# Kernel tuning notes

Hardware: AMD Instinct MI355X
Metric: run time of the kernel (lower is better)

Reference implementation:

```python
import jax, jax.numpy as jnp
import numpy as np

B, T, U = 64, 256, 256
NMEL, PRE, EMB, NF, ENC, DEC, WM, VOCAB = 80, 128, 15, 128, 128, 512, 10, 44
KMAX = 5
_km = np.zeros((3, KMAX), np.float32)
for _i, _k in enumerate([1, 3, 5]):
    _km[_i, (KMAX - _k) // 2:(KMAX - _k) // 2 + _k] = 1.0
KMASK = jnp.asarray(_km)  # [3, KMAX] zero-mask embedding kernels 1/3/5 in width-5 buffers


def _lstm(x, h, c, W, b):
    z = jnp.concatenate([x, h], -1) @ W + b
    i, f, g, o = jnp.split(z, 4, -1)
    cn = jax.nn.sigmoid(f) * c + jax.nn.sigmoid(i) * jnp.tanh(g)
    hn = jax.nn.sigmoid(o) * jnp.tanh(cn)
    return hn, cn


def _conv_stack(x, w, b, residual):
    # x [B,U,Cin]; w [3,KMAX,Cin,NF]; b [3,NF]; multi-kernel-size conv1d stack
    y = 0.0
    for i in range(3):
        wk = w[i] * KMASK[i][:, None, None]
        y = y + jax.lax.conv_general_dilated(x, wk, (1,), 'SAME', dimension_numbers=('NWC', 'WIO', 'NWC')) + b[i]
    y = jax.nn.relu(y)
    return y + x if residual else y


def _forward(text, in_mels, in_mel_mask, text_mask, w_pre1, b_pre1, w_pre2, b_pre2, emb, conv_w0, conv_b0, conv_w1, conv_b1, conv_w2, conv_b2, w_bif, b_bif, w_bib, b_bib, w_attlstm, b_attlstm, w_attproj, b_attproj, w_rnn1, b_rnn1, w_rnn2, b_rnn2, w_out, b_out):
    # mel prenet (two linear layers, dropout keep-prob 1.0 -> identity)
    corr = (in_mels @ w_pre1 + b_pre1) @ w_pre2 + b_pre2  # [T,B,PRE]
    # text encoder: embedding -> conv1d stack -> BiLSTM
    x = jnp.transpose(emb[text], (1, 0, 2))  # [B,U,EMB]
    x = _conv_stack(x, conv_w0, conv_b0, False)
    x = _conv_stack(x, conv_w1, conv_b1, True)
    x = _conv_stack(x, conv_w2, conv_b2, True)
    conv_text = jnp.transpose(x, (1, 0, 2))  # [U,B,NF]
    tm = text_mask[..., None]  # [U,B,1]

    def make_bi(W, bb):
        def f(carry, xs):
            h, c = carry
            xt, mt = xs
            hn, cn = _lstm(xt, h, c, W, bb)
            hn = mt * hn + (1.0 - mt) * h
            cn = mt * cn + (1.0 - mt) * c
            return (hn, cn), hn
        return f

    z0 = (jnp.zeros((B, ENC), jnp.float32), jnp.zeros((B, ENC), jnp.float32))
    _, hf = jax.lax.scan(make_bi(w_bif, b_bif), z0, (conv_text, tm))
    _, hb = jax.lax.scan(make_bi(w_bib, b_bib), z0, (conv_text[::-1], tm[::-1]))
    ctx = jnp.concatenate([hf, hb[::-1]], -1)  # [U,B,2*ENC]

    upos = jnp.arange(U, dtype=jnp.float32)[None, :, None]  # [1,U,1]
    phi_mask = text_mask.T  # [B,U]

    def step(carry, xs):
        att_w, att_k, att_h, att_c, h1, c1, h2, c2 = carry
        corr_t, m_t = xs
        m = m_t[:, None]
        # Gaussian-mixture attention cell (Graves-style, softplus step op)
        ah, ac = _lstm(jnp.concatenate([corr_t, att_w], -1), att_h, att_c, w_attlstm, b_attlstm)
        pr = ah @ w_attproj + b_attproj  # [B,3*WM]
        a_h, b_h, k_h = jnp.split(pr, 3, -1)
        a_t = jax.nn.softplus(a_h)
        b_t = jax.nn.softplus(b_h)
        k_t = att_k + jax.nn.softplus(k_h)  # attention_scale = 1.0
        phi = (a_t[:, None, :] * jnp.exp(-b_t[:, None, :] * (k_t[:, None, :] - upos) ** 2)).sum(-1) * phi_mask  # [B,U]
        w_t = jnp.einsum('bu,ubd->bd', phi, ctx)
        w_t = m * w_t + (1.0 - m) * att_w
        k_t = m * k_t + (1.0 - m) * att_k
        ah = m * ah + (1.0 - m) * att_h
        ac = m * ac + (1.0 - m) * att_c
        h1n, c1n = _lstm(jnp.concatenate([corr_t, w_t, ah], -1), h1, c1, w_rnn1, b_rnn1)
        h1n = m * h1n + (1.0 - m) * h1
        c1n = m * c1n + (1.0 - m) * c1
        h2n, c2n = _lstm(jnp.concatenate([corr_t, w_t, h1n], -1), h2, c2, w_rnn2, b_rnn2)
        h2n = m * h2n + (1.0 - m) * h2
        c2n = m * c2n + (1.0 - m) * c2
        return (w_t, k_t, ah, ac, h1n, c1n, h2n, c2n), h2n

    zf = lambda d: jnp.zeros((B, d), jnp.float32)
    init = (zf(2 * ENC), zf(WM), zf(DEC), zf(DEC), zf(DEC), zf(DEC), zf(DEC), zf(DEC))
    _, outs = jax.lax.scan(step, init, (corr, in_mel_mask))  # outs [T,B,DEC]
    return outs @ w_out + b_out  # [T,B,NMEL]


def setup_inputs():
    key = jax.random.key(0)
    ks = iter(jax.random.split(key, 40))

    def w(shape, s=0.08):
        return jax.random.normal(next(ks), shape, jnp.float32) * s

    z = lambda *s: jnp.zeros(s, jnp.float32)
    return {
        'in_mels': jax.random.normal(next(ks), (T, B, NMEL), jnp.float32),
        'in_mel_mask': jnp.ones((T, B), jnp.float32),
        'text': jax.random.randint(next(ks), (U, B), 0, VOCAB),
        'text_mask': jnp.ones((U, B), jnp.float32),
        'w_pre1': w((NMEL, PRE)), 'b_pre1': z(PRE),
        'w_pre2': w((PRE, PRE)), 'b_pre2': z(PRE),
        'emb': w((VOCAB, EMB), 1.0),
        'conv_w0': w((3, KMAX, EMB, NF)), 'conv_b0': z(3, NF),
        'conv_w1': w((3, KMAX, NF, NF)), 'conv_b1': z(3, NF),
        'conv_w2': w((3, KMAX, NF, NF)), 'conv_b2': z(3, NF),
        'w_bif': w((NF + ENC, 4 * ENC)), 'b_bif': z(4 * ENC),
        'w_bib': w((NF + ENC, 4 * ENC)), 'b_bib': z(4 * ENC),
        'w_attlstm': w((PRE + 2 * ENC + DEC, 4 * DEC)), 'b_attlstm': z(4 * DEC),
        'w_attproj': w((DEC, 3 * WM)), 'b_attproj': z(3 * WM),
        'w_rnn1': w((PRE + 2 * ENC + 2 * DEC, 4 * DEC)), 'b_rnn1': z(4 * DEC),
        'w_rnn2': w((PRE + 2 * ENC + 2 * DEC, 4 * DEC)), 'b_rnn2': z(4 * DEC),
        'w_out': w((DEC, NMEL)), 'b_out': z(NMEL),
    }


def reference(in_mels, in_mel_mask, text, text_mask, w_pre1, b_pre1, w_pre2, b_pre2, emb, conv_w0, conv_b0, conv_w1, conv_b1, conv_w2, conv_b2, w_bif, b_bif, w_bib, b_bib, w_attlstm, b_attlstm, w_attproj, b_attproj, w_rnn1, b_rnn1, w_rnn2, b_rnn2, w_out, b_out):
    return _forward(text, in_mels, in_mel_mask, text_mask, w_pre1, b_pre1, w_pre2, b_pre2, emb, conv_w0, conv_b0, conv_w1, conv_b1, conv_w2, conv_b2, w_bif, b_bif, w_bib, b_bib, w_attlstm, b_attlstm, w_attproj, b_attproj, w_rnn1, b_rnn1, w_rnn2, b_rnn2, w_out, b_out)
```

## Files before the change

### kernel.cpp

```cpp
#include <hip/hip_runtime.h>
#include <math.h>

constexpr int NB    = 64;
constexpr int NT    = 256;
constexpr int NU    = 256;
constexpr int NMELc = 80;
constexpr int PREc  = 128;
constexpr int EMBc  = 15;
constexpr int NFc   = 128;
constexpr int ENCc  = 128;
constexpr int DECc  = 512;
constexpr int WMc   = 10;
constexpr int AKS   = 16;
constexpr size_t WSZ = (size_t)116 * 128 * 512;

using bf16x8 = __attribute__((ext_vector_type(8))) short;
using us8    = __attribute__((ext_vector_type(8))) unsigned short;
using f32x4  = __attribute__((ext_vector_type(4))) float;

__device__ __forceinline__ float sigm(float x) { return 1.0f / (1.0f + expf(-x)); }
__device__ __forceinline__ float softplusf(float x) { return fmaxf(x, 0.0f) + log1pf(expf(-fabsf(x))); }
__device__ __forceinline__ unsigned short f2bf(float f) {
  unsigned u = __builtin_bit_cast(unsigned, f);
  return (unsigned short)((u + 0x7FFFu + ((u >> 16) & 1u)) >> 16);
}
__device__ __forceinline__ float bf2f(unsigned short h) {
  return __builtin_bit_cast(float, (unsigned)h << 16);
}
__device__ __forceinline__ float ldF(const float* p) {
  return __hip_atomic_load(p, __ATOMIC_RELAXED, __HIP_MEMORY_SCOPE_AGENT);
}
__device__ __forceinline__ void stF(float* p, float v) {
  __hip_atomic_store(p, v, __ATOMIC_RELAXED, __HIP_MEMORY_SCOPE_AGENT);
}
__device__ __forceinline__ float2 ldF2(const float* p) {
  unsigned long long u = __hip_atomic_load((const unsigned long long*)p, __ATOMIC_RELAXED,
                                           __HIP_MEMORY_SCOPE_AGENT);
  return __builtin_bit_cast(float2, u);
}
__device__ __forceinline__ unsigned ldU(const unsigned* p) {
  return __hip_atomic_load(p, __ATOMIC_RELAXED, __HIP_MEMORY_SCOPE_AGENT);
}
__device__ __forceinline__ void stU(unsigned* p, unsigned v) {
  __hip_atomic_store(p, v, __ATOMIC_RELAXED, __HIP_MEMORY_SCOPE_AGENT);
}

template <int K, int N, int RB>
__global__ void k_dense(const float* __restrict__ X, const float* __restrict__ W,
                        const float* __restrict__ bias, float* __restrict__ Y, int R) {
  __shared__ float xs[RB][K];
  int r0 = blockIdx.x * RB;
  int tid = threadIdx.x;
  for (int idx = tid; idx < RB * K; idx += 128) {
    int r = idx / K, k = idx % K;
    xs[r][k] = (r0 + r < R) ? X[(size_t)(r0 + r) * K + k] : 0.0f;
  }
  __syncthreads();
  int j = tid;
  if (j >= N) return;
  float acc[RB];
#pragma unroll
  for (int r = 0; r < RB; ++r) acc[r] = 0.f;
  for (int k = 0; k < K; ++k) {
    float w = W[(size_t)k * N + j];
#pragma unroll
    for (int r = 0; r < RB; ++r) acc[r] += xs[r][k] * w;
  }
  float bj = bias[j];
  for (int r = 0; r < RB; ++r)
    if (r0 + r < R) Y[(size_t)(r0 + r) * N + j] = acc[r] + bj;
}

__global__ void k_embed(const int* __restrict__ text, const float* __restrict__ emb,
                        float* __restrict__ out) {
  int idx = blockIdx.x * blockDim.x + threadIdx.x;
  if (idx >= NB * NU * EMBc) return;
  int c = idx % EMBc;
  int bu = idx / EMBc;
  int u = bu % NU, b = bu / NU;
  out[idx] = emb[text[u * NB + b] * EMBc + c];
}

template <int CIN>
__global__ void k_weff(const float* __restrict__ w, const float* __restrict__ bb,
                       float* __restrict__ weff, float* __restrict__ beff) {
  int idx = blockIdx.x * blockDim.x + threadIdx.x;
  const int tot = 5 * CIN * NFc;
  if (idx < tot) {
    int f = idx % NFc;
    int tc = idx / NFc;
    int c = tc % CIN, t = tc / CIN;
// ... 120 lines not shown
      __syncthreads();
    }
    int upos = d ? (NU - 1 - u) : u;
#pragma unroll
    for (int e = 0; e < 2; ++e) {
      int idx = 2 * tid + e;
      int bi = idx >> 7, j = idx & 127;
      int b = b0 + bi;
      float zi = zs[bi][j], zf = zs[bi][128 + j], zg = zs[bi][256 + j], zo = zs[bi][384 + j];
      float cp = creg[e], hp = hs[bi][j];
      float cn = sigm(zf) * cp + sigm(zi) * tanhf(zg);
      float hn = sigm(zo) * tanhf(cn);
      float mt = text_mask[upos * NB + b];
      hn = mt * hn + (1.f - mt) * hp;
      cn = mt * cn + (1.f - mt) * cp;
      creg[e] = cn;
      hs[bi][j] = hn;
      ctx[((size_t)upos * NB + b) * 256 + d * 128 + j] = hn;
    }
    __syncthreads();
  }
}

__global__ __launch_bounds__(256) void k_wcvt(const float* __restrict__ w1,
                                              const float* __restrict__ wa,
                                              const float* __restrict__ w2,
                                              unsigned short* __restrict__ Wpk) {
  int ktg = blockIdx.x;
  int ntg = blockIdx.y;
  const float* W;
  int ktl;
  if (ktg < 44) { W = w1; ktl = ktg; }
  else if (ktg < 72) { W = wa; ktl = ktg - 44; }
  else { W = w2; ktl = ktg - 72; }
  int tid = threadIdx.x;
  for (int p = 0; p < 8; ++p) {
    int idx = p * 256 + tid;
    int ntl = idx >> 6, l = idx & 63;
    int nt = ntg * 32 + ntl;
    us8 vh, vl;
#pragma unroll
    for (int j = 0; j < 8; ++j) {
      float wv = W[(size_t)(ktl * 32 + (l >> 4) * 8 + j) * 2048 + nt * 16 + (l & 15)];
      unsigned short h = f2bf(wv);
      vh[j] = h;
      vl[j] = f2bf(wv - bf2f(h));
    }
    size_t o = (((size_t)ktg * 128 + nt) * 64 + l) * 8;
    *(us8*)(Wpk + o) = vh;
    *(us8*)(Wpk + WSZ + o) = vl;
  }
}

struct DecMp {
  const float* corr;
  const unsigned short* Wpk;
  const float *mel_mask, *text_mask, *ctx;
  const float *b_att, *b_rnn1, *b_rnn2, *w_proj, *b_proj;
  float *aw, *ak, *ah, *ac, *h1, *c1, *c2, *outs, *zerob;
  float* zX;
  unsigned* flags;
};

__device__ __forceinline__ void wait_flags(const unsigned* flags, int base, unsigned target) {
  int tid = threadIdx.x;
  for (;;) {
    bool ok = true;
    if (tid < 128) {
      int f = (tid < 64) ? (base + tid) : (192 + base + (tid - 64));
      ok = (ldU(&flags[f]) >= target);
    }
    if (__syncthreads_and(ok)) break;
    __builtin_amdgcn_s_sleep(8);
  }
}

__device__ __forceinline__ void do_gateM(const float* zX, int clo, int chi, const float* bias,
                                         const float* cprev, const float* hprev, bool zfirst,
                                         const float* mm, float* hout, float* cout, int b, int j) {
  float2 zi = *(const float2*)(bias + j);
  float2 zf = *(const float2*)(bias + 512 + j);
  float2 zg = *(const float2*)(bias + 1024 + j);
  float2 zo = *(const float2*)(bias + 1536 + j);
  for (int c = clo; c <= chi; ++c) {
    const float* q = zX + ((size_t)c * NB + b) * 2048 + j;
    float2 a = ldF2(q), f2 = ldF2(q + 512), g2 = ldF2(q + 1024), o2 = ldF2(q + 1536);
    zi.x += a.x; zi.y += a.y;
    zf.x += f2.x; zf.y += f2.y;
    zg.x += g2.x; zg.y += g2.y;
    zo.x += o2.x; zo.y += o2.y;
  }
  float2 cp = zfirst ? make_float2(0.f, 0.f) : *(const float2*)(cprev + (size_t)b * 512 + j);
  float2 hp = zfirst ? make_float2(0.f, 0.f) : *(const float2*)(hprev + (size_t)b * 512 + j);
  float m = mm[b];
  float cnx = sigm(zf.x) * cp.x + sigm(zi.x) * tanhf(zg.x);
  float cny = sigm(zf.y) * cp.y + sigm(zi.y) * tanhf(zg.y);
  float hnx = sigm(zo.x) * tanhf(cnx);
  float hny = sigm(zo.y) * tanhf(cny);
  *(float2*)(hout + (size_t)b * 512 + j) =
      make_float2(m * hnx + (1.f - m) * hp.x, m * hny + (1.f - m) * hp.y);
  *(float2*)(cout + (size_t)b * 512 + j) =
      make_float2(m * cnx + (1.f - m) * cp.x, m * cny + (1.f - m) * cp.y);
}

__global__ __launch_bounds__(256) void k_decM(DecMp P, int i) {
  __shared__ __align__(16) unsigned short xsh[32][360];
  __shared__ __align__(16) unsigned short xsl[32][360];
  int tid = threadIdx.x, bid = blockIdx.x;
  if (bid < 384) {
    int bg = bid / 192, r = bid % 192, c = r >> 4, nc = r & 15;
    int g, ktg0, nkt, k0;
    if (c < 4)      { g = 0; ktg0 = c * 11;            nkt = 11; k0 = c * 352; }
    else if (c < 8) { g = 1; ktg0 = 44 + (c - 4) * 7;  nkt = 7;  k0 = (c - 4) * 224; }
    else            { g = 2; ktg0 = 72 + (c - 8) * 11; nkt = 11; k0 = (c - 8) * 352; }
    int s = (g == 0) ? (i - 1) : (g == 1 ? i : (i - 2));
    if (s >= 0 && s < NT) {
      const float* p0 = P.corr + (size_t)s * NB * PREc;
      const float *p1, *p2, *p3;
      int s1, s2_, s3;
      if (g == 1) {
        bool z = (s == 0);
        int pp = (s - 1) & 1;
        p1 = z ? P.zerob : P.aw + (size_t)pp * NB * 256; s1 = z ? 0 : 256;
        p2 = z ? P.zerob : P.ah + (size_t)pp * NB * DECc; s2_ = z ? 0 : DECc;
        p3 = P.zerob; s3 = 0;
      } else if (g == 0) {
        int pp = s & 1;
        p1 = P.aw + (size_t)pp * NB * 256; s1 = 256;
        p2 = P.ah + (size_t)pp * NB * DECc; s2_ = DECc;
        bool z = (s == 0);
        p3 = z ? P.zerob : P.h1 + (size_t)((s - 1) & 1) * NB * DECc; s3 = z ? 0 : DECc;
      } else {
        int pp = s & 1;
        p1 = P.aw + (size_t)pp * NB * 256; s1 = 256;
        p2 = P.h1 + (size_t)pp * NB * DECc; s2_ = DECc;
        bool z = (s == 0);
        p3 = z ? P.zerob : P.outs + (size_t)(s - 1) * NB * DECc; s3 = z ? 0 : DECc;
      }
      int klen = nkt * 32;
      for (int idx = tid; idx < klen; idx += 256) {
        int k = k0 + idx;
#pragma unroll 4
        for (int bi = 0; bi < 32; ++bi) {
          int b = bg * 32 + bi;
          float v;
          int kx = k;
          if (kx < PREc)
            v = p0[(size_t)b * PREc + kx];
          else {
            kx -= PREc;
            if (kx < 256)
              v = p1[(size_t)b * s1 + kx];
            else {
              kx -= 256;
              if (kx < DECc)
                v = p2[(size_t)b * s2_ + kx];
              else
                v = p3[(size_t)b * s3 + (kx - DECc)];
            }
          }
          unsigned short h = f2bf(v);
          xsh[bi][idx] = h;
          xsl[bi][idx] = f2bf(v - bf2f(h));
        }
      }
      __syncthreads();
      int w = tid >> 6, lane = tid & 63;
      const unsigned short* wb0 =
          P.Wpk + (((size_t)ktg0 * 128 + (size_t)(nc * 8 + w * 2)) * 64 + lane) * 8;
      f32x4 acc[2][2];
#pragma unroll
      for (int m = 0; m < 2; ++m)
#pragma unroll
        for (int t = 0; t < 2; ++t) acc[m][t] = f32x4{0.f, 0.f, 0.f, 0.f};
      int arow0 = lane & 15, acol = (lane >> 4) * 8;
      for (int kt = 0; kt < nkt; ++kt) {
        bf16x8 ah0 = *(const bf16x8*)&xsh[arow0][kt * 32 + acol];
        bf16x8 ah1 = *(const bf16x8*)&xsh[16 + arow0][kt * 32 + acol];
        bf16x8 al0 = *(const bf16x8*)&xsl[arow0][kt * 32 + acol];
        bf16x8 al1 = *(const bf16x8*)&xsl[16 + arow0][kt * 32 + acol];
        const unsigned short* wp = wb0 + (size_t)kt * 65536;
        bf16x8 b0h = *(const bf16x8*)(wp);
        bf16x8 b1h = *(const bf16x8*)(wp + 512);
        bf16x8 b0l = *(const bf16x8*)(wp + WSZ);
        bf16x8 b1l = *(const bf16x8*)(wp + WSZ + 512);
        acc[0][0] = __builtin_amdgcn_mfma_f32_16x16x32_bf16(ah0, b0h, acc[0][0], 0, 0, 0);
        acc[0][1] = __builtin_amdgcn_mfma_f32_16x16x32_bf16(ah0, b1h, acc[0][1], 0, 0, 0);
        acc[1][0] = __builtin_amdgcn_mfma_f32_16x16x32_bf16(ah1, b0h, acc[1][0], 0, 0, 0);
        acc[1][1] = __builtin_amdgcn_mfma_f32_16x16x32_bf16(ah1, b1h, acc[1][1], 0, 0, 0);
        acc[0][0] = __builtin_amdgcn_mfma_f32_16x16x32_bf16(al0, b0h, acc[0][0], 0, 0, 0);
        acc[0][1] = __builtin_amdgcn_mfma_f32_16x16x32_bf16(al0, b1h, acc[0][1], 0, 0, 0);
        acc[1][0] = __builtin_amdgcn_mfma_f32_16x16x32_bf16(al1, b0h, acc[1][0], 0, 0, 0);
        acc[1][1] = __builtin_amdgcn_mfma_f32_16x16x32_bf16(al1, b1h, acc[1][1], 0, 0, 0);
        acc[0][0] = __builtin_amdgcn_mfma_f32_16x16x32_bf16(ah0, b0l, acc[0][0], 0, 0, 0);
        acc[0][1] = __builtin_amdgcn_mfma_f32_16x16x32_bf16(ah0, b1l, acc[0][1], 0, 0, 0);
        acc[1][0] = __builtin_amdgcn_mfma_f32_16x16x32_bf16(ah1, b0l, acc[1][0], 0, 0, 0);
        acc[1][1] = __builtin_amdgcn_mfma_f32_16x16x32_bf16(ah1, b1l, acc[1][1], 0, 0, 0);
      }
#pragma unroll
      for (int m = 0; m < 2; ++m)
#pragma unroll
        for (int t = 0; t < 2; ++t) {
          int brow = bg * 32 + m * 16 + (lane >> 4) * 4;
          int col = nc * 128 + (w * 2 + t) * 16 + (lane & 15);
          float* zb = P.zX + ((size_t)c * NB + brow) * 2048 + col;
#pragma unroll
          for (int rr = 0; rr < 4; ++rr) stF(zb + (size_t)rr * 2048, acc[m][t][rr]);
        }
    }
    __syncthreads();
    if (tid == 0) stU(&P.flags[bid], (unsigned)(i + 1));
    return;
  }
  int wb = bid - 384;
  unsigned target = (unsigned)(i + 1);
  if (wb < 64) {
    int s = i - 1;
    if (s < 0 || s >= NT) return;
    wait_flags(P.flags, 0, target);
    bool z = (s == 0);
    do_gateM(P.zX, 0, 3, P.b_rnn1,
             z ? P.zerob : P.c1 + (size_t)((s - 1) & 1) * NB * 512,
             z ? P.zerob : P.h1 + (size_t)((s - 1) & 1) * NB * 512, z,
             P.mel_mask + (size_t)s * NB,
             P.h1 + (size_t)(s & 1) * NB * 512,
             P.c1 + (size_t)(s & 1) * NB * 512, wb, 2 * tid);
    return;
  }
  if (wb < 128) {
    int s = i - 2;
    if (s < 0 || s >= NT) return;
    wait_flags(P.flags, 128, target);
    bool z = (s == 0);
    do_gateM(P.zX, 8, 11, P.b_rnn2,
             z ? P.zerob : P.c2 + (size_t)((s - 1) & 1) * NB * 512,
             z ? P.zerob : P.outs + (size_t)(s - 1) * NB * 512, z,
             P.mel_mask + (size_t)s * NB,
             P.outs + (size_t)s * NB * 512,
             P.c2 + (size_t)(s & 1) * NB * 512, wb - 64, 2 * tid);
    return;
  }
  int s = i;
  if (s >= NT) return;
  wait_flags(P.flags, 64, target);
  int b = wb - 128;
  float* sh = (float*)&xsh[0][0];
  float* ah_s = sh;
  float* red_s = sh + 512;
  float* pr_s = sh + 768;
  float* abk = sh + 800;
  float* phi_s = sh + 896;
  float m = P.mel_mask[(size_t)s * NB + b];
  bool z = (s == 0);
  int pp = (s - 1) & 1;
  {
    int j = 2 * tid;
    float2 zi = *(const float2*)(P.b_att + j);
    float2 zf = *(const float2*)(P.b_att + 512 + j);
    float2 zg = *(const float2*)(P.b_att + 1024 + j);
    float2 zo = *(const float2*)(P.b_att + 1536 + j);
    for (int cc = 4; cc <= 7; ++cc) {
      const float* q = P.zX + ((size_t)cc * NB + b) * 2048 + j;
      float2 a = ldF2(q), f2 = ldF2(q + 512), g2 = ldF2(q + 1024), o2 = ldF2(q + 1536);
      zi.x += a.x; zi.y += a.y;
      zf.x += f2.x; zf.y += f2.y;
      zg.x += g2.x; zg.y += g2.y;
      zo.x += o2.x; zo.y += o2.y;
    }
    float2 cp = z ? make_float2(0.f, 0.f)
                  : *(const float2*)(P.ac + (size_t)pp * NB * 512 + (size_t)b * 512 + j);
    float2 hp = z ? make_float2(0.f, 0.f)
                  : *(const float2*)(P.ah + (size_t)pp * NB * 512 + (size_t)b * 512 + j);
    float cnx = sigm(zf.x) * cp.x + sigm(zi.x) * tanhf(zg.x);
    float cny = sigm(zf.y) * cp.y + sigm(zi.y) * tanhf(zg.y);
    float hrx = sigm(zo.x) * tanhf(cnx);
    float hry = sigm(zo.y) * tanhf(cny);
    ah_s[j] = hrx;
    ah_s[j + 1] = hry;
    *(float2*)(P.ah + (size_t)(s & 1) * NB * 512 + (size_t)b * 512 + j) =
        make_float2(m * hrx + (1.f - m) * hp.x, m * hry + (1.f - m) * hp.y);
    *(float2*)(P.ac + (size_t)(s & 1) * NB * 512 + (size_t)b * 512 + j) =
        make_float2(m * cnx + (1.f - m) * cp.x, m * cny + (1.f - m) * cp.y);
  }
  __syncthreads();
  {
    int cc2 = tid & 31, ch = tid >> 5;
    float ssum = 0.f;
    if (cc2 < 30)
      for (int k = ch * 64; k < ch * 64 + 64; ++k) ssum += ah_s[k] * P.w_proj[k * 30 + cc2];
    red_s[ch * 32 + cc2] = ssum;
  }
  __syncthreads();
  if (tid < 30) {
    float ssum = P.b_proj[tid];
    for (int ch = 0; ch < 8; ++ch) ssum += red_s[ch * 32 + tid];
    pr_s[tid] = ssum;
  }
  __syncthreads();
  if (tid < WMc) {
    float kp = z ? 0.f : P.ak[(size_t)pp * NB * AKS + (size_t)b * AKS + tid];
    float a_t = softplusf(pr_s[tid]);
    float b_t = softplusf(pr_s[WMc + tid]);
    float k_t = kp + softplusf(pr_s[2 * WMc + tid]);
    abk[tid] = a_t;
    abk[32 + tid] = b_t;
    abk[64 + tid] = k_t;
    P.ak[(size_t)(s & 1) * NB * AKS + (size_t)b * AKS + tid] = m * k_t + (1.f - m) * kp;
  }
  __syncthreads();
  {
    int u = tid;
    float ssum = 0.f;
#pragma unroll
    for (int gg = 0; gg < WMc; ++gg) {
      float dd = abk[64 + gg] - (float)u;
      ssum += abk[gg] * expf(-abk[32 + gg] * dd * dd);
    }
    phi_s[u] = ssum * P.text_mask[u * NB + b];
  }
  __syncthreads();
  {
    int dcol = tid;
    float ssum = 0.f;
#pragma unroll 8
    for (int u = 0; u < NU; ++u)
      ssum += phi_s[u] * __builtin_nontemporal_load(P.ctx + ((size_t)u * NB + b) * 256 + dcol);
    float wprev = z ? 0.f : P.aw[(size_t)pp * NB * 256 + (size_t)b * 256 + dcol];
    P.aw[(size_t)(s & 1) * NB * 256 + (size_t)b * 256 + dcol] = m * ssum + (1.f - m) * wprev;
  }
}

extern "C" void kernel_launch(void* const* d_in, const int* in_sizes, int n_in,
                              void* d_out, int out_size, void* d_ws, size_t ws_size,
                              hipStream_t stream) {
  const float* in_mels = (const float*)d_in[0];
  const float* mel_mask = (const float*)d_in[1];
  const int* text = (const int*)d_in[2];
  const float* text_mask = (const float*)d_in[3];
  const float* w_pre1 = (const float*)d_in[4];
  const float* b_pre1 = (const float*)d_in[5];
  const float* w_pre2 = (const float*)d_in[6];
  const float* b_pre2 = (const float*)d_in[7];
  const float* emb = (const float*)d_in[8];
  const float* conv_w0 = (const float*)d_in[9];
  const float* conv_b0 = (const float*)d_in[10];
  const float* conv_w1 = (const float*)d_in[11];
  const float* conv_b1 = (const float*)d_in[12];
  const float* conv_w2 = (const float*)d_in[13];
  const float* conv_b2 = (const float*)d_in[14];
  const float* w_bif = (const float*)d_in[15];
  const float* b_bif = (const float*)d_in[16];
  const float* w_bib = (const float*)d_in[17];
  const float* b_bib = (const float*)d_in[18];
  const float* w_att = (const float*)d_in[19];
  const float* b_att = (const float*)d_in[20];
  const float* w_proj = (const float*)d_in[21];
  const float* b_proj = (const float*)d_in[22];
  const float* w_rnn1 = (const float*)d_in[23];
  const float* b_rnn1 = (const float*)d_in[24];
  const float* w_rnn2 = (const float*)d_in[25];
  const float* b_rnn2 = (const float*)d_in[26];
  const float* w_outp = (const float*)d_in[27];
  const float* b_outp = (const float*)d_in[28];

  float* ws = (float*)d_ws;
  size_t off = 0;
  auto alloc = [&](size_t n) {
    float* p = ws + off;
    off += (n + 63) & ~(size_t)63;
    return p;
  };
  float* corr = alloc((size_t)NT * NB * PREc);
  float* embx = alloc((size_t)NB * NU * EMBc);
  float* wpkR = alloc(WSZ);
  float* zX = alloc((size_t)12 * NB * 2048);
  float* ctx = alloc((size_t)NU * NB * 2 * ENCc);
  float* convbuf = alloc((size_t)NB * NU * NFc);
  float* aw = alloc((size_t)2 * NB * 2 * ENCc);
  float* ak = alloc((size_t)2 * NB * AKS);
  float* ah = alloc((size_t)2 * NB * DECc);
  float* ac = alloc((size_t)2 * NB * DECc);
  float* h1 = alloc((size_t)2 * NB * DECc);
  float* c1 = alloc((size_t)2 * NB * DECc);
  float* c2 = alloc((size_t)2 * NB * DECc);
  float* outs = alloc((size_t)NT * NB * DECc);
  float* weff0 = alloc((size_t)5 * EMBc * NFc);
  float* beff0 = alloc(NFc);
  float* weff1 = alloc((size_t)5 * NFc * NFc);
  float* beff1 = alloc(NFc);
  float* weff2 = alloc((size_t)5 * NFc * NFc);
  float* beff2 = alloc(NFc);
  float* zerob = alloc(1024);
  float* flagsf = alloc(512);
  unsigned* flags = (unsigned*)flagsf;

  unsigned short* Wpk = (unsigned short*)wpkR;
  _Float16* zx = (_Float16*)outs;
  float* tmp = wpkR;
  float* convA = wpkR;
  float* convB = ctx;

  hipMemsetAsync(zerob, 0, 1024 * sizeof(float), stream);
  hipMemsetAsync(flags, 0, 512 * sizeof(unsigned), stream);

  k_dense<NMELc, PREc, 8><<<NT * NB / 8, 128, 0, stream>>>(in_mels, w_pre1, b_pre1, tmp, NT * NB);
  k_dense<PREc, PREc, 8><<<NT * NB / 8, 128, 0, stream>>>(tmp, w_pre2, b_pre2, corr, NT * NB);

  k_embed<<<(NB * NU * EMBc + 255) / 256, 256, 0, stream>>>(text, emb, embx);
  k_weff<EMBc><<<(5 * EMBc * NFc + 255) / 256, 256, 0, stream>>>(conv_w0, conv_b0, weff0, beff0);
  k_weff<NFc><<<(5 * NFc * NFc + 255) / 256, 256, 0, stream>>>(conv_w1, conv_b1, weff1, beff1);
  k_weff<NFc><<<(5 * NFc * NFc + 255) / 256, 256, 0, stream>>>(conv_w2, conv_b2, weff2, beff2);
  k_conv<EMBc, false><<<dim3(NU / 8, NB), 128, 0, stream>>>(embx, weff0, beff0, convB);
  k_conv<NFc, true><<<dim3(NU / 8, NB), 128, 0, stream>>>(convB, weff1, beff1, convA);
  k_conv<NFc, true><<<dim3(NU / 8, NB), 128, 0, stream>>>(convA, weff2, beff2, convbuf);

  k_wcvt<<<dim3(116, 4), 256, 0, stream>>>(w_rnn1, w_att, w_rnn2, Wpk);

  k_zx<<<dim3(512, 8), 512, 0, stream>>>(w_bif, b_bif, w_bib, b_bib, convbuf, zx);
  k_encP2<<<32, 256, 0, stream>>>(w_bif, w_bib, zx, text_mask, ctx);

  DecMp M;
  M.corr = corr; M.Wpk = Wpk;
  M.mel_mask = mel_mask; M.text_mask = text_mask; M.ctx = ctx;
  M.b_att = b_att; M.b_rnn1 = b_rnn1; M.b_rnn2 = b_rnn2;
  M.w_proj = w_proj; M.b_proj = b_proj;
  M.aw = aw; M.ak = ak; M.ah = ah; M.ac = ac;
  M.h1 = h1; M.c1 = c1; M.c2 = c2; M.outs = outs; M.zerob = zerob;
  M.zX = zX; M.flags = flags;
  for (int i = 0; i <= NT + 1; ++i) {
    k_decM<<<576, 256, 0, stream>>>(M, i);
  }

  k_dense<DECc, NMELc, 8><<<NT * NB / 8, 128, 0, stream>>>(outs, w_outp, b_outp, (float*)d_out,
                                                           NT * NB);
}
```

Before: 13.05 ms.

## Replace per-step decoder launches with one persistent kernel using flag-based sync

The 258 separate decoder kernel launches are folded into a single persistent kernel of 512 blocks. Each block loops over all timesteps and coordinates with per-batch-group and per-batch flags in global memory. GEMM blocks, gate blocks (rnn1 and rnn2 merged into one block per batch row) and attention blocks each spin on the producer flags they depend on. This removes launch overhead and inter-kernel bubbles, but needs every block co-resident (launch_bounds with 2 blocks per CU) and adds spin-wait and atomic-load traffic.

```diff
diff --git a/kernel.cpp b/kernel.cpp
--- a/kernel.cpp
+++ b/kernel.cpp
@@ -37,6 +37,10 @@
   unsigned long long u = __hip_atomic_load((const unsigned long long*)p, __ATOMIC_RELAXED,
                                            __HIP_MEMORY_SCOPE_AGENT);
   return __builtin_bit_cast(float2, u);
+}
+__device__ __forceinline__ void stF2(float* p, float2 v) {
+  __hip_atomic_store((unsigned long long*)p, __builtin_bit_cast(unsigned long long, v),
+                     __ATOMIC_RELAXED, __HIP_MEMORY_SCOPE_AGENT);
 }
 __device__ __forceinline__ unsigned ldU(const unsigned* p) {
   return __hip_atomic_load(p, __ATOMIC_RELAXED, __HIP_MEMORY_SCOPE_AGENT);
@@ -263,58 +267,17 @@
   }
 }
 
-struct DecMp {
+struct DecPp {
   const float* corr;
   const unsigned short* Wpk;
   const float *mel_mask, *text_mask, *ctx;
   const float *b_att, *b_rnn1, *b_rnn2, *w_proj, *b_proj;
   float *aw, *ak, *ah, *ac, *h1, *c1, *c2, *outs, *zerob;
   float* zX;
-  unsigned* flags;
+  unsigned *fa, *fbatt, *fbg;
 };
 
-__device__ __forceinline__ void wait_flags(const unsigned* flags, int base, unsigned target) {
-  int tid = threadIdx.x;
-  for (;;) {
-    bool ok = true;
-    if (tid < 128) {
-      int f = (tid < 64) ? (base + tid) : (192 + base + (tid - 64));
-      ok = (ldU(&flags[f]) >= target);
-    }
-    if (__syncthreads_and(ok)) break;
-    __builtin_amdgcn_s_sleep(8);
-  }
-}
-
-__device__ __forceinline__ void do_gateM(const float* zX, int clo, int chi, const float* bias,
-                                         const float* cprev, const float* hprev, bool zfirst,
-                                         const float* mm, float* hout, float* cout, int b, int j) {
-  float2 zi = *(const float2*)(bias + j);
-  float2 zf = *(const float2*)(bias + 512 + j);
-  float2 zg = *(const float2*)(bias + 1024 + j);
-  float2 zo = *(const float2*)(bias + 1536 + j);
-  for (int c = clo; c <= chi; ++c) {
-    const float* q = zX + ((size_t)c * NB + b) * 2048 + j;
-    float2 a = ldF2(q), f2 = ldF2(q + 512), g2 = ldF2(q + 1024), o2 = ldF2(q + 1536);
-    zi.x += a.x; zi.y += a.y;
-    zf.x += f2.x; zf.y += f2.y;
-    zg.x += g2.x; zg.y += g2.y;
-    zo.x += o2.x; zo.y += o2.y;
-  }
-  float2 cp = zfirst ? make_float2(0.f, 0.f) : *(const float2*)(cprev + (size_t)b * 512 + j);
-  float2 hp = zfirst ? make_float2(0.f, 0.f) : *(const float2*)(hprev + (size_t)b * 512 + j);
-  float m = mm[b];
-  float cnx = sigm(zf.x) * cp.x + sigm(zi.x) * tanhf(zg.x);
-  float cny = sigm(zf.y) * cp.y + sigm(zi.y) * tanhf(zg.y);
-  float hnx = sigm(zo.x) * tanhf(cnx);
-  float hny = sigm(zo.y) * tanhf(cny);
-  *(float2*)(hout + (size_t)b * 512 + j) =
-      make_float2(m * hnx + (1.f - m) * hp.x, m * hny + (1.f - m) * hp.y);
-  *(float2*)(cout + (size_t)b * 512 + j) =
-      make_float2(m * cnx + (1.f - m) * cp.x, m * cny + (1.f - m) * cp.y);
-}
-
-__global__ __launch_bounds__(256) void k_decM(DecMp P, int i) {
+__global__ __launch_bounds__(256, 2) void k_decP3(DecPp P) {
   __shared__ __align__(16) unsigned short xsh[32][360];
   __shared__ __align__(16) unsigned short xsl[32][360];
   int tid = threadIdx.x, bid = blockIdx.x;
@@ -324,220 +287,302 @@
     if (c < 4)      { g = 0; ktg0 = c * 11;            nkt = 11; k0 = c * 352; }
     else if (c < 8) { g = 1; ktg0 = 44 + (c - 4) * 7;  nkt = 7;  k0 = (c - 4) * 224; }
     else            { g = 2; ktg0 = 72 + (c - 8) * 11; nkt = 11; k0 = (c - 8) * 352; }
-    int s = (g == 0) ? (i - 1) : (g == 1 ? i : (i - 2));
-    if (s >= 0 && s < NT) {
-      const float* p0 = P.corr + (size_t)s * NB * PREc;
-      const float *p1, *p2, *p3;
-      int s1, s2_, s3;
-      if (g == 1) {
-        bool z = (s == 0);
-        int pp = (s - 1) & 1;
-        p1 = z ? P.zerob : P.aw + (size_t)pp * NB * 256; s1 = z ? 0 : 256;
-        p2 = z ? P.zerob : P.ah + (size_t)pp * NB * DECc; s2_ = z ? 0 : DECc;
-        p3 = P.zerob; s3 = 0;
-      } else if (g == 0) {
-        int pp = s & 1;
-        p1 = P.aw + (size_t)pp * NB * 256; s1 = 256;
-        p2 = P.ah + (size_t)pp * NB * DECc; s2_ = DECc;
-        bool z = (s == 0);
-        p3 = z ? P.zerob : P.h1 + (size_t)((s - 1) & 1) * NB * DECc; s3 = z ? 0 : DECc;
-      } else {
-        int pp = s & 1;
-        p1 = P.aw + (size_t)pp * NB * 256; s1 = 256;
-        p2 = P.h1 + (size_t)pp * NB * DECc; s2_ = DECc;
-        bool z = (s == 0);
-        p3 = z ? P.zerob : P.outs + (size_t)(s - 1) * NB * DECc; s3 = z ? 0 : DECc;
-      }
-      int klen = nkt * 32;
-      for (int idx = tid; idx < klen; idx += 256) {
-        int k = k0 + idx;
+    int b0 = bg * 32;
+    int w = tid >> 6, lane = tid & 63;
+    const unsigned short* wb0 =
+        P.Wpk + (((size_t)ktg0 * 128 + (size_t)(nc * 8 + w * 2)) * 64 + lane) * 8;
+    int arow0 = lane & 15, acol = (lane >> 4) * 8;
+    for (int i = 0; i <= NT + 1; ++i) {
+      unsigned ta, tg;
+      if (g == 0)      { ta = (unsigned)i; tg = (unsigned)i; }
+      else if (g == 1) { ta = (unsigned)i; tg = 0u; }
+      else             { ta = (i > 0) ? (unsigned)(i - 1) : 0u; tg = (unsigned)i; }
+      for (;;) {
+        bool ok = true;
+        if (tid < 32) ok = (ldU(&P.fbatt[b0 + tid]) >= ta);
+        else if (tid < 64) ok = (ldU(&P.fbg[b0 + tid - 32]) >= tg);
+        if (__syncthreads_and(ok)) break;
+        __builtin_amdgcn_s_sleep(16);
+      }
+      int s = (g == 0) ? (i - 1) : (g == 1 ? i : (i - 2));
+      if (s >= 0 && s < NT) {
+        const float* p0 = P.corr + (size_t)s * NB * PREc;
+        const float *p1, *p2, *p3;
+        int s1, s2_, s3;
+        if (g == 1) {
+          bool z = (s == 0);
+          int pp = (s - 1) & 1;
+          p1 = z ? P.zerob : P.aw + (size_t)pp * NB * 256; s1 = z ? 0 : 256;
+          p2 = z ? P.zerob : P.ah + (size_t)pp * NB * DECc; s2_ = z ? 0 : DECc;
+          p3 = P.zerob; s3 = 0;
+        } else if (g == 0) {
+          int pp = s & 1;
+          p1 = P.aw + (size_t)pp * NB * 256; s1 = 256;
+          p2 = P.ah + (size_t)pp * NB * DECc; s2_ = DECc;
+          bool z = (s == 0);
+          p3 = z ? P.zerob : P.h1 + (size_t)((s - 1) & 1) * NB * DECc; s3 = z ? 0 : DECc;
+        } else {
+          int pp = s & 1;
+          p1 = P.aw + (size_t)pp * NB * 256; s1 = 256;
+          p2 = P.h1 + (size_t)pp * NB * DECc; s2_ = DECc;
+          bool z = (s == 0);
+          p3 = z ? P.zerob : P.outs + (size_t)(s - 1) * NB * DECc; s3 = z ? 0 : DECc;
+        }
+        int klen = nkt * 32;
+        for (int idx = tid; idx < klen; idx += 256) {
+          int k = k0 + idx;
 #pragma unroll 4
-        for (int bi = 0; bi < 32; ++bi) {
-          int b = bg * 32 + bi;
-          float v;
-          int kx = k;
-          if (kx < PREc)
-            v = p0[(size_t)b * PREc + kx];
-          else {
-            kx -= PREc;
-            if (kx < 256)
-              v = p1[(size_t)b * s1 + kx];
+          for (int bi = 0; bi < 32; ++bi) {
+            int b = b0 + bi;
+            float v;
+            int kx = k;
+            if (kx < PREc)
+              v = p0[(size_t)b * PREc + kx];
             else {
-              kx -= 256;
-              if (kx < DECc)
-                v = p2[(size_t)b * s2_ + kx];
-              else
-                v = p3[(size_t)b * s3 + (kx - DECc)];
+              kx -= PREc;
+              if (kx < 256)
+                v = ldF(p1 + (size_t)b * s1 + kx);
+              else {
+                kx -= 256;
+                if (kx < DECc)
+                  v = ldF(p2 + (size_t)b * s2_ + kx);
+                else
+                  v = ldF(p3 + (size_t)b * s3 + (kx - DECc));
+              }
             }
+            unsigned short h = f2bf(v);
+            xsh[bi][idx] = h;
+            xsl[bi][idx] = f2bf(v - bf2f(h));
           }
-          unsigned short h = f2bf(v);
-          xsh[bi][idx] = h;
-          xsl[bi][idx] = f2bf(v - bf2f(h));
-        }
-      }
-      __syncthreads();
-      int w = tid >> 6, lane = tid & 63;
-      const unsigned short* wb0 =
-          P.Wpk + (((size_t)ktg0 * 128 + (size_t)(nc * 8 + w * 2)) * 64 + lane) * 8;
-      f32x4 acc[2][2];
-#pragma unroll
-      for (int m = 0; m < 2; ++m)
-#pragma unroll
-        for (int t = 0; t < 2; ++t) acc[m][t] = f32x4{0.f, 0.f, 0.f, 0.f};
-      int arow0 = lane & 15, acol = (lane >> 4) * 8;
-      for (int kt = 0; kt < nkt; ++kt) {
-        bf16x8 ah0 = *(const bf16x8*)&xsh[arow0][kt * 32 + acol];
-        bf16x8 ah1 = *(const bf16x8*)&xsh[16 + arow0][kt * 32 + acol];
-        bf16x8 al0 = *(const bf16x8*)&xsl[arow0][kt * 32 + acol];
-        bf16x8 al1 = *(const bf16x8*)&xsl[16 + arow0][kt * 32 + acol];
-        const unsigned short* wp = wb0 + (size_t)kt * 65536;
-        bf16x8 b0h = *(const bf16x8*)(wp);
-        bf16x8 b1h = *(const bf16x8*)(wp + 512);
-        bf16x8 b0l = *(const bf16x8*)(wp + WSZ);
-        bf16x8 b1l = *(const bf16x8*)(wp + WSZ + 512);
-        acc[0][0] = __builtin_amdgcn_mfma_f32_16x16x32_bf16(ah0, b0h, acc[0][0], 0, 0, 0);
-        acc[0][1] = __builtin_amdgcn_mfma_f32_16x16x32_bf16(ah0, b1h, acc[0][1], 0, 0, 0);
-        acc[1][0] = __builtin_amdgcn_mfma_f32_16x16x32_bf16(ah1, b0h, acc[1][0], 0, 0, 0);
-        acc[1][1] = __builtin_amdgcn_mfma_f32_16x16x32_bf16(ah1, b1h, acc[1][1], 0, 0, 0);
-        acc[0][0] = __builtin_amdgcn_mfma_f32_16x16x32_bf16(al0, b0h, acc[0][0], 0, 0, 0);
-        acc[0][1] = __builtin_amdgcn_mfma_f32_16x16x32_bf16(al0, b1h, acc[0][1], 0, 0, 0);
-        acc[1][0] = __builtin_amdgcn_mfma_f32_16x16x32_bf16(al1, b0h, acc[1][0], 0, 0, 0);
-        acc[1][1] = __builtin_amdgcn_mfma_f32_16x16x32_bf16(al1, b1h, acc[1][1], 0, 0, 0);
-        acc[0][0] = __builtin_amdgcn_mfma_f32_16x16x32_bf16(ah0, b0l, acc[0][0], 0, 0, 0);
-        acc[0][1] = __builtin_amdgcn_mfma_f32_16x16x32_bf16(ah0, b1l, acc[0][1], 0, 0, 0);
-        acc[1][0] = __builtin_amdgcn_mfma_f32_16x16x32_bf16(ah1, b0l, acc[1][0], 0, 0, 0);
-        acc[1][1] = __builtin_amdgcn_mfma_f32_16x16x32_bf16(ah1, b1l, acc[1][1], 0, 0, 0);
-      }
-#pragma unroll
-      for (int m = 0; m < 2; ++m)
-#pragma unroll
-        for (int t = 0; t < 2; ++t) {
-          int brow = bg * 32 + m * 16 + (lane >> 4) * 4;
-          int col = nc * 128 + (w * 2 + t) * 16 + (lane & 15);
-          float* zb = P.zX + ((size_t)c * NB + brow) * 2048 + col;
-#pragma unroll
-          for (int rr = 0; rr < 4; ++rr) stF(zb + (size_t)rr * 2048, acc[m][t][rr]);
-        }
+        }
+        __syncthreads();
+        f32x4 acc[2][2];
+#pragma unroll
+        for (int m = 0; m < 2; ++m)
+#pragma unroll
+          for (int t = 0; t < 2; ++t) acc[m][t] = f32x4{0.f, 0.f, 0.f, 0.f};
+        for (int kt = 0; kt < nkt; ++kt) {
+          bf16x8 ah0 = *(const bf16x8*)&xsh[arow0][kt * 32 + acol];
+          bf16x8 ah1 = *(const bf16x8*)&xsh[16 + arow0][kt * 32 + acol];
+          bf16x8 al0 = *(const bf16x8*)&xsl[arow0][kt * 32 + acol];
+          bf16x8 al1 = *(const bf16x8*)&xsl[16 + arow0][kt * 32 + acol];
+          const unsigned short* wp = wb0 + (size_t)kt * 65536;
+          bf16x8 b0h = *(const bf16x8*)(wp);
+          bf16x8 b1h = *(const bf16x8*)(wp + 512);
+          bf16x8 b0l = *(const bf16x8*)(wp + WSZ);
+          bf16x8 b1l = *(const bf16x8*)(wp + WSZ + 512);
+          acc[0][0] = __builtin_amdgcn_mfma_f32_16x16x32_bf16(ah0, b0h, acc[0][0], 0, 0, 0);
+          acc[0][1] = __builtin_amdgcn_mfma_f32_16x16x32_bf16(ah0, b1h, acc[0][1], 0, 0, 0);
+          acc[1][0] = __builtin_amdgcn_mfma_f32_16x16x32_bf16(ah1, b0h, acc[1][0], 0, 0, 0);
+          acc[1][1] = __builtin_amdgcn_mfma_f32_16x16x32_bf16(ah1, b1h, acc[1][1], 0, 0, 0);
+          acc[0][0] = __builtin_amdgcn_mfma_f32_16x16x32_bf16(al0, b0h, acc[0][0], 0, 0, 0);
+          acc[0][1] = __builtin_amdgcn_mfma_f32_16x16x32_bf16(al0, b1h, acc[0][1], 0, 0, 0);
+          acc[1][0] = __builtin_amdgcn_mfma_f32_16x16x32_bf16(al1, b0h, acc[1][0], 0, 0, 0);
+          acc[1][1] = __builtin_amdgcn_mfma_f32_16x16x32_bf16(al1, b1h, acc[1][1], 0, 0, 0);
+          acc[0][0] = __builtin_amdgcn_mfma_f32_16x16x32_bf16(ah0, b0l, acc[0][0], 0, 0, 0);
+          acc[0][1] = __builtin_amdgcn_mfma_f32_16x16x32_bf16(ah0, b1l, acc[0][1], 0, 0, 0);
+          acc[1][0] = __builtin_amdgcn_mfma_f32_16x16x32_bf16(ah1, b0l, acc[1][0], 0, 0, 0);
+          acc[1][1] = __builtin_amdgcn_mfma_f32_16x16x32_bf16(ah1, b1l, acc[1][1], 0, 0, 0);
+        }
+#pragma unroll
+        for (int m = 0; m < 2; ++m)
+#pragma unroll
+          for (int t = 0; t < 2; ++t) {
+            int brow = b0 + m * 16 + (lane >> 4) * 4;
+            int col = nc * 128 + (w * 2 + t) * 16 + (lane & 15);
+            float* zb = P.zX + ((size_t)c * NB + brow) * 2048 + col;
+#pragma unroll
+            for (int rr = 0; rr < 4; ++rr) stF(zb + (size_t)rr * 2048, acc[m][t][rr]);
+          }
+      }
+      __syncthreads();
+      if (tid == 0) stU(&P.fa[bid], (unsigned)(i + 1));
+    }
+    return;
+  }
+  int wb = bid - 384;
+  if (wb < 64) {
+    int b = wb;
+    int bg = b >> 5;
+    for (int i = 0; i <= NT + 1; ++i) {
+      for (;;) {
+        bool ok = true;
+        if (tid < 128) {
+          int idx = tid >> 4;
+          int cc = (idx < 4) ? idx : (idx + 4);
+          ok = (ldU(&P.fa[bg * 192 + cc * 16 + (tid & 15)]) >= (unsigned)(i + 1));
+        }
+        if (__syncthreads_and(ok)) break;
+        __builtin_amdgcn_s_sleep(16);
+      }
+      int j = 2 * tid;
+      {
+        int s = i - 1;
+        if (s >= 0 && s < NT) {
+          bool z = (s == 0);
+          const float* cprev = z ? P.zerob : P.c1 + (size_t)((s - 1) & 1) * NB * 512;
+          const float* hprev = z ? P.zerob : P.h1 + (size_t)((s - 1) & 1) * NB * 512;
+          float2 zi = *(const float2*)(P.b_rnn1 + j);
+          float2 zf = *(const float2*)(P.b_rnn1 + 512 + j);
+          float2 zg = *(const float2*)(P.b_rnn1 + 1024 + j);
+          float2 zo = *(const float2*)(P.b_rnn1 + 1536 + j);
+          for (int cc = 0; cc <= 3; ++cc) {
+            const float* q = P.zX + ((size_t)cc * NB + b) * 2048 + j;
+            float2 a = ldF2(q), f2 = ldF2(q + 512), g2 = ldF2(q + 1024), o2 = ldF2(q + 1536);
+            zi.x += a.x; zi.y += a.y;
+            zf.x += f2.x; zf.y += f2.y;
+            zg.x += g2.x; zg.y += g2.y;
+            zo.x += o2.x; zo.y += o2.y;
+          }
+          float2 cp = z ? make_float2(0.f, 0.f) : ldF2(cprev + (size_t)b * 512 + j);
+          float2 hp = z ? make_float2(0.f, 0.f) : ldF2(hprev + (size_t)b * 512 + j);
+          float m = P.mel_mask[(size_t)s * NB + b];
+          float cnx = sigm(zf.x) * cp.x + sigm(zi.x) * tanhf(zg.x);
+          float cny = sigm(zf.y) * cp.y + sigm(zi.y) * tanhf(zg.y);
+          float hnx = sigm(zo.x) * tanhf(cnx);
+          float hny = sigm(zo.y) * tanhf(cny);
+          stF2(P.h1 + (size_t)(s & 1) * NB * 512 + (size_t)b * 512 + j,
+               make_float2(m * hnx + (1.f - m) * hp.x, m * hny + (1.f - m) * hp.y));
+          stF2(P.c1 + (size_t)(s & 1) * NB * 512 + (size_t)b * 512 + j,
+               make_float2(m * cnx + (1.f - m) * cp.x, m * cny + (1.f - m) * cp.y));
+        }
+      }
+      {
+        int s = i - 2;
+        if (s >= 0 && s < NT) {
+          bool z = (s == 0);
+          const float* cprev = z ? P.zerob : P.c2 + (size_t)((s - 1) & 1) * NB * 512;
+          const float* hprev = z ? P.zerob : P.outs + (size_t)(s - 1) * NB * 512;
+          float2 zi = *(const float2*)(P.b_rnn2 + j);
+          float2 zf = *(const float2*)(P.b_rnn2 + 512 + j);
+          float2 zg = *(const float2*)(P.b_rnn2 + 1024 + j);
+          float2 zo = *(const float2*)(P.b_rnn2 + 1536 + j);
+          for (int cc = 8; cc <= 11; ++cc) {
+            const float* q = P.zX + ((size_t)cc * NB + b) * 2048 + j;
+            float2 a = ldF2(q), f2 = ldF2(q + 512), g2 = ldF2(q + 1024), o2 = ldF2(q + 1536);
+            zi.x += a.x; zi.y += a.y;
+            zf.x += f2.x; zf.y += f2.y;
+            zg.x += g2.x; zg.y += g2.y;
+            zo.x += o2.x; zo.y += o2.y;
+          }
+          float2 cp = z ? make_float2(0.f, 0.f) : ldF2(cprev + (size_t)b * 512 + j);
+          float2 hp = z ? make_float2(0.f, 0.f) : ldF2(hprev + (size_t)b * 512 + j);
+          float m = P.mel_mask[(size_t)s * NB + b];
+          float cnx = sigm(zf.x) * cp.x + sigm(zi.x) * tanhf(zg.x);
+          float cny = sigm(zf.y) * cp.y + sigm(zi.y) * tanhf(zg.y);
+          float hnx = sigm(zo.x) * tanhf(cnx);
+          float hny = sigm(zo.y) * tanhf(cny);
+          stF2(P.outs + (size_t)s * NB * 512 + (size_t)b * 512 + j,
+               make_float2(m * hnx + (1.f - m) * hp.x, m * hny + (1.f - m) * hp.y));
+          stF2(P.c2 + (size_t)(s & 1) * NB * 512 + (size_t)b * 512 + j,
+               make_float2(m * cnx + (1.f - m) * cp.x, m * cny + (1.f - m) * cp.y));
+        }
+      }
+      __syncthreads();
+      if (tid == 0) stU(&P.fbg[b], (unsigned)(i + 1));
+    }
+    return;
+  }
+  int b = wb - 64;
+  int bg = b >> 5;
+  float* sh = (float*)&xsh[0][0];
+  for (int i = 0; i <= NT + 1; ++i) {
+    for (;;) {
+      bool ok = true;
+      if (tid < 64)
+        ok = (ldU(&P.fa[bg * 192 + (4 + (tid >> 4)) * 16 + (tid & 15)]) >= (unsigned)(i + 1));
+      if (__syncthreads_and(ok)) break;
+      __builtin_amdgcn_s_sleep(16);
+    }
+    int s = i;
+    if (s < NT) {
+      float* ah_s = sh;
+      float* red_s = sh + 512;
+      float* pr_s = sh + 768;
+      float* abk = sh + 800;
+      float* phi_s = sh + 896;
+      float m = P.mel_mask[(size_t)s * NB + b];
+      bool z = (s == 0);
+      int pp = (s - 1) & 1;
+      {
+        int j = 2 * tid;
+        float2 zi = *(const float2*)(P.b_att + j);
+        float2 zf = *(const float2*)(P.b_att + 512 + j);
+        float2 zg = *(const float2*)(P.b_att + 1024 + j);
+        float2 zo = *(const float2*)(P.b_att + 1536 + j);
+        for (int cc = 4; cc <= 7; ++cc) {
+          const float* q = P.zX + ((size_t)cc * NB + b) * 2048 + j;
+          float2 a = ldF2(q), f2 = ldF2(q + 512), g2 = ldF2(q + 1024), o2 = ldF2(q + 1536);
+          zi.x += a.x; zi.y += a.y;
+          zf.x += f2.x; zf.y += f2.y;
+          zg.x += g2.x; zg.y += g2.y;
+          zo.x += o2.x; zo.y += o2.y;
+        }
+        float2 cp = z ? make_float2(0.f, 0.f)
+                      : ldF2(P.ac + (size_t)pp * NB * 512 + (size_t)b * 512 + j);
+        float2 hp = z ? make_float2(0.f, 0.f)
+                      : ldF2(P.ah + (size_t)pp * NB * 512 + (size_t)b * 512 + j);
+        float cnx = sigm(zf.x) * cp.x + sigm(zi.x) * tanhf(zg.x);
+        float cny = sigm(zf.y) * cp.y + sigm(zi.y) * tanhf(zg.y);
+        float hrx = sigm(zo.x) * tanhf(cnx);
+        float hry = sigm(zo.y) * tanhf(cny);
+        ah_s[j] = hrx;
+        ah_s[j + 1] = hry;
+        stF2(P.ah + (size_t)(s & 1) * NB * 512 + (size_t)b * 512 + j,
+             make_float2(m * hrx + (1.f - m) * hp.x, m * hry + (1.f - m) * hp.y));
+        stF2(P.ac + (size_t)(s & 1) * NB * 512 + (size_t)b * 512 + j,
+             make_float2(m * cnx + (1.f - m) * cp.x, m * cny + (1.f - m) * cp.y));
+      }
+      __syncthreads();
+      {
+        int cc2 = tid & 31, ch = tid >> 5;
+        float ssum = 0.f;
+        if (cc2 < 30)
+          for (int k = ch * 64; k < ch * 64 + 64; ++k) ssum += ah_s[k] * P.w_proj[k * 30 + cc2];
+        red_s[ch * 32 + cc2] = ssum;
+      }
+      __syncthreads();
+      if (tid < 30) {
+        float ssum = P.b_proj[tid];
+        for (int ch = 0; ch < 8; ++ch) ssum += red_s[ch * 32 + tid];
+        pr_s[tid] = ssum;
+      }
+      __syncthreads();
+      if (tid < WMc) {
+        float kp = z ? 0.f : ldF(P.ak + (size_t)pp * NB * AKS + (size_t)b * AKS + tid);
+        float a_t = softplusf(pr_s[tid]);
+        float b_t = softplusf(pr_s[WMc + tid]);
+        float k_t = kp + softplusf(pr_s[2 * WMc + tid]);
+        abk[tid] = a_t;
+        abk[32 + tid] = b_t;
+        abk[64 + tid] = k_t;
+        stF(P.ak + (size_t)(s & 1) * NB * AKS + (size_t)b * AKS + tid, m * k_t + (1.f - m) * kp);
+      }
+      __syncthreads();
+      {
+        int u = tid;
+        float ssum = 0.f;
+#pragma unroll
+        for (int gg = 0; gg < WMc; ++gg) {
+          float dd = abk[64 + gg] - (float)u;
+          ssum += abk[gg] * expf(-abk[32 + gg] * dd * dd);
+        }
+        phi_s[u] = ssum * P.text_mask[u * NB + b];
+      }
+      __syncthreads();
+      {
+        int dcol = tid;
+        float ssum = 0.f;
+#pragma unroll 8
+        for (int u = 0; u < NU; ++u)
+          ssum += phi_s[u] * __builtin_nontemporal_load(P.ctx + ((size_t)u * NB + b) * 256 + dcol);
+        float wprev = z ? 0.f : ldF(P.aw + (size_t)pp * NB * 256 + (size_t)b * 256 + dcol);
+        stF(P.aw + (size_t)(s & 1) * NB * 256 + (size_t)b * 256 + dcol,
+            m * ssum + (1.f - m) * wprev);
+      }
     }
     __syncthreads();
-    if (tid == 0) stU(&P.flags[bid], (unsigned)(i + 1));
-    return;
-  }
-  int wb = bid - 384;
-  unsigned target = (unsigned)(i + 1);
-  if (wb < 64) {
-    int s = i - 1;
-    if (s < 0 || s >= NT) return;
-    wait_flags(P.flags, 0, target);
-    bool z = (s == 0);
-    do_gateM(P.zX, 0, 3, P.b_rnn1,
-             z ? P.zerob : P.c1 + (size_t)((s - 1) & 1) * NB * 512,
-             z ? P.zerob : P.h1 + (size_t)((s - 1) & 1) * NB * 512, z,
-             P.mel_mask + (size_t)s * NB,
-             P.h1 + (size_t)(s & 1) * NB * 512,
-             P.c1 + (size_t)(s & 1) * NB * 512, wb, 2 * tid);
-    return;
-  }
-  if (wb < 128) {
-    int s = i - 2;
-    if (s < 0 || s >= NT) return;
-    wait_flags(P.flags, 128, target);
-    bool z = (s == 0);
-    do_gateM(P.zX, 8, 11, P.b_rnn2,
-             z ? P.zerob : P.c2 + (size_t)((s - 1) & 1) * NB * 512,
-             z ? P.zerob : P.outs + (size_t)(s - 1) * NB * 512, z,
-             P.mel_mask + (size_t)s * NB,
-             P.outs + (size_t)s * NB * 512,
-             P.c2 + (size_t)(s & 1) * NB * 512, wb - 64, 2 * tid);
-    return;
-  }
-  int s = i;
-  if (s >= NT) return;
-  wait_flags(P.flags, 64, target);
-  int b = wb - 128;
-  float* sh = (float*)&xsh[0][0];
-  float* ah_s = sh;
-  float* red_s = sh + 512;
-  float* pr_s = sh + 768;
-  float* abk = sh + 800;
-  float* phi_s = sh + 896;
-  float m = P.mel_mask[(size_t)s * NB + b];
-  bool z = (s == 0);
-  int pp = (s - 1) & 1;
-  {
-    int j = 2 * tid;
-    float2 zi = *(const float2*)(P.b_att + j);
-    float2 zf = *(const float2*)(P.b_att + 512 + j);
-    float2 zg = *(const float2*)(P.b_att + 1024 + j);
-    float2 zo = *(const float2*)(P.b_att + 1536 + j);
-    for (int cc = 4; cc <= 7; ++cc) {
-      const float* q = P.zX + ((size_t)cc * NB + b) * 2048 + j;
-      float2 a = ldF2(q), f2 = ldF2(q + 512), g2 = ldF2(q + 1024), o2 = ldF2(q + 1536);
-      zi.x += a.x; zi.y += a.y;
-      zf.x += f2.x; zf.y += f2.y;
-      zg.x += g2.x; zg.y += g2.y;
-      zo.x += o2.x; zo.y += o2.y;
-    }
-    float2 cp = z ? make_float2(0.f, 0.f)
-                  : *(const float2*)(P.ac + (size_t)pp * NB * 512 + (size_t)b * 512 + j);
-    float2 hp = z ? make_float2(0.f, 0.f)
-                  : *(const float2*)(P.ah + (size_t)pp * NB * 512 + (size_t)b * 512 + j);
-    float cnx = sigm(zf.x) * cp.x + sigm(zi.x) * tanhf(zg.x);
-    float cny = sigm(zf.y) * cp.y + sigm(zi.y) * tanhf(zg.y);
-    float hrx = sigm(zo.x) * tanhf(cnx);
-    float hry = sigm(zo.y) * tanhf(cny);
-    ah_s[j] = hrx;
-    ah_s[j + 1] = hry;
-    *(float2*)(P.ah + (size_t)(s & 1) * NB * 512 + (size_t)b * 512 + j) =
-        make_float2(m * hrx + (1.f - m) * hp.x, m * hry + (1.f - m) * hp.y);
-    *(float2*)(P.ac + (size_t)(s & 1) * NB * 512 + (size_t)b * 512 + j) =
-        make_float2(m * cnx + (1.f - m) * cp.x, m * cny + (1.f - m) * cp.y);
-  }
-  __syncthreads();
-  {
-    int cc2 = tid & 31, ch = tid >> 5;
-    float ssum = 0.f;
-    if (cc2 < 30)
-      for (int k = ch * 64; k < ch * 64 + 64; ++k) ssum += ah_s[k] * P.w_proj[k * 30 + cc2];
-    red_s[ch * 32 + cc2] = ssum;
-  }
-  __syncthreads();
-  if (tid < 30) {
-    float ssum = P.b_proj[tid];
-    for (int ch = 0; ch < 8; ++ch) ssum += red_s[ch * 32 + tid];
-    pr_s[tid] = ssum;
-  }
-  __syncthreads();
-  if (tid < WMc) {
-    float kp = z ? 0.f : P.ak[(size_t)pp * NB * AKS + (size_t)b * AKS + tid];
-    float a_t = softplusf(pr_s[tid]);
-    float b_t = softplusf(pr_s[WMc + tid]);
-    float k_t = kp + softplusf(pr_s[2 * WMc + tid]);
-    abk[tid] = a_t;
-    abk[32 + tid] = b_t;
-    abk[64 + tid] = k_t;
-    P.ak[(size_t)(s & 1) * NB * AKS + (size_t)b * AKS + tid] = m * k_t + (1.f - m) * kp;
-  }
-  __syncthreads();
-  {
-    int u = tid;
-    float ssum = 0.f;
-#pragma unroll
-    for (int gg = 0; gg < WMc; ++gg) {
-      float dd = abk[64 + gg] - (float)u;
-      ssum += abk[gg] * expf(-abk[32 + gg] * dd * dd);
-    }
-    phi_s[u] = ssum * P.text_mask[u * NB + b];
-  }
-  __syncthreads();
-  {
-    int dcol = tid;
-    float ssum = 0.f;
-#pragma unroll 8
-    for (int u = 0; u < NU; ++u)
-      ssum += phi_s[u] * __builtin_nontemporal_load(P.ctx + ((size_t)u * NB + b) * 256 + dcol);
-    float wprev = z ? 0.f : P.aw[(size_t)pp * NB * 256 + (size_t)b * 256 + dcol];
-    P.aw[(size_t)(s & 1) * NB * 256 + (size_t)b * 256 + dcol] = m * ssum + (1.f - m) * wprev;
+    if (tid == 0) stU(&P.fbatt[b], (unsigned)(i + 1));
   }
 }
 
@@ -602,8 +647,10 @@
   float* weff2 = alloc((size_t)5 * NFc * NFc);
   float* beff2 = alloc(NFc);
   float* zerob = alloc(1024);
-  float* flagsf = alloc(512);
-  unsigned* flags = (unsigned*)flagsf;
+  float* flagsf = alloc(1024);
+  unsigned* fa = (unsigned*)flagsf;
+  unsigned* fbatt = fa + 448;
+  unsigned* fbg = fa + 512;
 
   unsigned short* Wpk = (unsigned short*)wpkR;
   _Float16* zx = (_Float16*)outs;
@@ -612,7 +659,7 @@
   float* convB = ctx;
 
   hipMemsetAsync(zerob, 0, 1024 * sizeof(float), stream);
-  hipMemsetAsync(flags, 0, 512 * sizeof(unsigned), stream);
+  hipMemsetAsync(flagsf, 0, 1024 * sizeof(float), stream);
 
   k_dense<NMELc, PREc, 8><<<NT * NB / 8, 128, 0, stream>>>(in_mels, w_pre1, b_pre1, tmp, NT * NB);
   k_dense<PREc, PREc, 8><<<NT * NB / 8, 128, 0, stream>>>(tmp, w_pre2, b_pre2, corr, NT * NB);
@@ -630,17 +677,16 @@
   k_zx<<<dim3(512, 8), 512, 0, stream>>>(w_bif, b_bif, w_bib, b_bib, convbuf, zx);
   k_encP2<<<32, 256, 0, stream>>>(w_bif, w_bib, zx, text_mask, ctx);
 
-  DecMp M;
-  M.corr = corr; M.Wpk = Wpk;
-  M.mel_mask = mel_mask; M.text_mask = text_mask; M.ctx = ctx;
-  M.b_att = b_att; M.b_rnn1 = b_rnn1; M.b_rnn2 = b_rnn2;
-  M.w_proj = w_proj; M.b_proj = b_proj;
-  M.aw = aw; M.ak = ak; M.ah = ah; M.ac = ac;
-  M.h1 = h1; M.c1 = c1; M.c2 = c2; M.outs = outs; M.zerob = zerob;
-  M.zX = zX; M.flags = flags;
-  for (int i = 0; i <= NT + 1; ++i) {
-    k_decM<<<576, 256, 0, stream>>>(M, i);
-  }
+  DecPp D;
+  D.corr = corr; D.Wpk = Wpk;
+  D.mel_mask = mel_mask; D.text_mask = text_mask; D.ctx = ctx;
+  D.b_att = b_att; D.b_rnn1 = b_rnn1; D.b_rnn2 = b_rnn2;
+  D.w_proj = w_proj; D.b_proj = b_proj;
+  D.aw = aw; D.ak = ak; D.ah = ah; D.ac = ac;
+  D.h1 = h1; D.c1 = c1; D.c2 = c2; D.outs = outs; D.zerob = zerob;
+  D.zX = zX;
+  D.fa = fa; D.fbatt = fbatt; D.fbg = fbg;
+  k_decP3<<<512, 256, 0, stream>>>(D);
 
   k_dense<DECc, NMELc, 8><<<NT * NB / 8, 128, 0, stream>>>(outs, w_outp, b_outp, (float*)d_out,
                                                            NT * NB);
```

Measured after the change: 17.76 ms. 36.1% more time.
